# Kernel tuning notes

Measured on AMD Instinct MI355X. Metric: run time of the kernel, lower is better.

## Reference

```python
import jax, jax.numpy as jnp
import numpy as np

D = 1024
H = 16
DK = D // H


def apply_rope(x):
    # x: [B, H, T, dk]; interleaved-pair RoPE as in the torch source
    T, dim = x.shape[-2], x.shape[-1]
    inv_freq = 1.0 / (10000.0 ** (jnp.arange(0, dim, 2, dtype=x.dtype) / dim))  # [dk/2]
    pos = jnp.arange(T, dtype=x.dtype)
    sinusoid = pos[:, None] * inv_freq[None, :]  # [T, dk/2]
    sin, cos = jnp.sin(sinusoid), jnp.cos(sinusoid)
    x1, x2 = x[..., ::2], x[..., 1::2]
    rot = jnp.stack([x1 * cos - x2 * sin, x1 * sin + x2 * cos], axis=-1)
    return rot.reshape(x.shape)


def setup_inputs() -> dict:
    key = jax.random.key(0)
    k1, k2, k3, k4, k5 = jax.random.split(key, 5)
    B, T = 2, 2048
    s = 1.0 / np.sqrt(D)
    return {
        "x": jax.random.normal(k1, (B, T, D), dtype=jnp.float32),
        "W_qkv": jax.random.normal(k2, (D, 3 * D), dtype=jnp.float32) * s,
        "b_qkv": jnp.zeros((3 * D,), dtype=jnp.float32),
        "W_out": jax.random.normal(k3, (D, D), dtype=jnp.float32) * s,
        "b_out": jnp.zeros((D,), dtype=jnp.float32),
    }


def reference(x, W_qkv, b_qkv, W_out, b_out):
    B, T, C = x.shape
    qkv = x @ W_qkv + b_qkv  # [B, T, 3D]
    qkv = qkv.reshape(B, T, 3, H, DK).transpose(2, 0, 3, 1, 4)  # [3, B, H, T, dk]
    q, k, v = qkv[0], qkv[1], qkv[2]
    q, k = apply_rope(q), apply_rope(k)
    scores = jnp.einsum("bhtd,bhsd->bhts", q, k) / jnp.sqrt(jnp.asarray(DK, x.dtype))
    causal = jnp.tril(jnp.ones((T, T), dtype=bool))
    scores = jnp.where(causal, scores, jnp.asarray(-1e9, x.dtype))
    probs = jax.nn.softmax(scores, axis=-1)
    attn = jnp.einsum("bhts,bhsd->bhtd", probs, v)  # [B, H, T, dk]
    out = attn.transpose(0, 2, 1, 3).reshape(B, T, C)  # b h t d -> b t (h d)
    return out @ W_out + b_out
```

## Files before the change

kernel.cpp:

```cpp
#include <hip/hip_runtime.h>
#include <math.h>

#define DMODEL 1024
#define NHEAD  16
#define HDK    64
#define BATCH  2
#define SEQ    2048
#define MROWS  (BATCH*SEQ)
#define NQKV   (3*DMODEL)
#define LOG2_10000 13.287712379549449f
#define INV2PI 0.15915494309189535f
#define SCALE_LOG2E 0.1803368801111137f
#define M_FIX 8.0f

typedef __attribute__((ext_vector_type(8))) short bf16x8;
typedef __attribute__((ext_vector_type(4))) float f32x4;

__device__ __forceinline__ short f2bf(float f) {
    union { float f; unsigned u; } v; v.f = f;
    unsigned r = v.u + 0x7fffu + ((v.u >> 16) & 1u);
    return (short)(r >> 16);
}

__device__ __forceinline__ float fast_exp2(float x) {
#if __has_builtin(__builtin_amdgcn_exp2f)
    return __builtin_amdgcn_exp2f(x);
#else
    return exp2f(x);
#endif
}

__device__ __forceinline__ void gld_lds16(const short* g, short* l) {
    __builtin_amdgcn_global_load_lds(
        (const __attribute__((address_space(1))) void*)g,
        (__attribute__((address_space(3))) void*)l, 16, 0, 0);
}

__global__ __launch_bounds__(256) void prep_kernel(
    const float* __restrict__ x, const float* __restrict__ wqkv,
    const float* __restrict__ wout,
    short* __restrict__ xb, short* __restrict__ wqkv_t, short* __restrict__ wout_t)
{
    __shared__ short tile[32][33];
    const int tid = threadIdx.x;
    if (blockIdx.x < 2048) {
        const int i = (blockIdx.x * 256 + tid) * 8;
        float4 a = *(const float4*)(x + i);
        float4 b = *(const float4*)(x + i + 4);
        bf16x8 o;
        o[0] = f2bf(a.x); o[1] = f2bf(a.y); o[2] = f2bf(a.z); o[3] = f2bf(a.w);
        o[4] = f2bf(b.x); o[5] = f2bf(b.y); o[6] = f2bf(b.z); o[7] = f2bf(b.w);
        *(bf16x8*)(xb + i) = o;
        return;
    }
    const int bx = blockIdx.x - 2048;
    int nx = bx & 127;
    const int ky = bx >> 7;
    const float* in; short* out; int N;
    if (nx < 96) { in = wqkv; out = wqkv_t; N = NQKV; }
    else         { in = wout; out = wout_t; N = DMODEL; nx -= 96; }
    const int tx = tid & 31, ty = tid >> 5;
    const int n0 = nx * 32, k0 = ky * 32;
    #pragma unroll
    for (int i = 0; i < 32; i += 8)
        tile[ty + i][tx] = f2bf(in[(size_t)(k0 + ty + i) * N + n0 + tx]);
    __syncthreads();
    #pragma unroll
    for (int i = 0; i < 32; i += 8)
        out[(size_t)(n0 + ty + i) * DMODEL + k0 + tx] = tile[tx][ty + i];
}

__global__ __launch_bounds__(256) void qkv_gemm_kernel(
    const short* __restrict__ xb, const short* __restrict__ Wt,
    const float* __restrict__ bias,
    short* __restrict__ qd, short* __restrict__ kd, short* __restrict__ vtb)
{
    __shared__ __align__(16) short As[128 * 32];
    __shared__ __align__(16) short Bs[128 * 32];
    const int tid = threadIdx.x;
    const int lane = tid & 63, wave = tid >> 6;
    const int wm = wave & 1, wn = wave >> 1;
    const int l15 = lane & 15, quad = lane >> 4;
    const int n0 = blockIdx.x * 128, m0 = blockIdx.y * 128;
    const int srow = lane >> 2, sc = lane & 3;

    const short* gA1 = xb + (size_t)(m0 + wave * 32 + srow) * DMODEL + sc * 8;
    const short* gA2 = gA1 + (size_t)16 * DMODEL;
    const short* gB1 = Wt + (size_t)(n0 + wave * 32 + srow) * DMODEL + sc * 8;
    const short* gB2 = gB1 + (size_t)16 * DMODEL;
    short* lA1 = As + (wave * 32) * 32;
    short* lA2 = As + (wave * 32 + 16) * 32;
    short* lB1 = Bs + (wave * 32) * 32;
    short* lB2 = Bs + (wave * 32 + 16) * 32;

    f32x4 zero = {0.f, 0.f, 0.f, 0.f};
    f32x4 acc[4][4];
    #pragma unroll
    for (int i = 0; i < 4; ++i)
        #pragma unroll
        for (int j = 0; j < 4; ++j) acc[i][j] = zero;

    for (int k0 = 0; k0 < DMODEL; k0 += 32) {
        __syncthreads();
        gld_lds16(gA1 + k0, lA1);
        gld_lds16(gA2 + k0, lA2);
        gld_lds16(gB1 + k0, lB1);
        gld_lds16(gB2 + k0, lB2);
        __syncthreads();
        bf16x8 af[4], bfr[4];
        #pragma unroll
        for (int i = 0; i < 4; ++i)
            af[i] = *(const bf16x8*)&As[(wm * 64 + i * 16 + l15) * 32 + quad * 8];
        #pragma unroll
        for (int j = 0; j < 4; ++j)
            bfr[j] = *(const bf16x8*)&Bs[(wn * 64 + j * 16 + l15) * 32 + quad * 8];
        #pragma unroll
        for (int i = 0; i < 4; ++i)
            #pragma unroll
            for (int j = 0; j < 4; ++j)
                acc[i][j] = __builtin_amdgcn_mfma_f32_16x16x32_bf16(af[i], bfr[j], acc[i][j], 0, 0, 0);
    }

    const int which = n0 >> 10;
    float biasv[4], invf[4];
    int hh[4], dd[4];
    #pragma unroll
    for (int j = 0; j < 4; ++j) {
        const int n = n0 + wn * 64 + j * 16 + l15;
        biasv[j] = bias[n];
        hh[j] = (n & 1023) >> 6;
        dd[j] = n & 63;
        invf[j] = INV2PI * exp2f(-((float)(dd[j] & ~1) / 64.f) * LOG2_10000);
    }
    #pragma unroll
    for (int i = 0; i < 4; ++i) {
        #pragma unroll
        for (int r = 0; r < 4; ++r) {
            const int m = m0 + wm * 64 + i * 16 + quad * 4 + r;
            const int b = m >> 11, t = m & (SEQ - 1);
            #pragma unroll
            for (int j = 0; j < 4; ++j) {
                float val = acc[i][j][r] + biasv[j];
                if (which < 2) {
                    const float rev = (float)t * invf[j];
                    const float fr = rev - floorf(rev);
                    const float s = __builtin_amdgcn_sinf(fr);
                    const float c = __builtin_amdgcn_cosf(fr);
                    const float partner = __shfl_xor(val, 1);
                    val = (lane & 1) ? (partner * s + val * c) : (val * c - partner * s);
                    short* dst = (which == 0) ? qd : kd;
                    dst[((size_t)(b * NHEAD + hh[j]) * SEQ + t) * HDK + dd[j]] = f2bf(val);
                } else {
                    vtb[((size_t)(b * NHEAD + hh[j]) * HDK + dd[j]) * SEQ + t] = f2bf(val);
                }
            }
        }
    }
}

__global__ __launch_bounds__(256) void attn_mfma_kernel(
    const short* __restrict__ qd, const short* __restrict__ kd,
    const short* __restrict__ vt, short* __restrict__ od)
{
    __shared__ __align__(16) short Ks[2][2][64 * 32];
    __shared__ __align__(16) short Vs[2][2][64 * 32];
    __shared__ __align__(16) short Ps[4][16][72];
    const int tid = threadIdx.x, lane = tid & 63, w = tid >> 6;
    const int l15 = lane & 15, quad = lane >> 4;
    const int id = (int)blockIdx.x;
    const int c = id & 7, kk = id >> 3;
    const int qp = kk & 15, jj = kk >> 4;
    const int hb = c + 8 * jj;
    const int h = hb & 15, b = hb >> 4;
    const size_t base = ((size_t)(b * NHEAD + h)) * SEQ * HDK;
    const int srow = tid >> 2, sc = tid & 3;
    const int lofs = tid * 8;
    f32x4 zero = {0.f, 0.f, 0.f, 0.f};

    const int qtile[2] = { qp, 31 - qp };
    const short* kp0 = kd + base + (size_t)srow * HDK + sc * 8;
    const short* vp0 = vt + base + (size_t)srow * SEQ + sc * 8;
    const short* kp1 = kp0 + (size_t)64 * HDK;
    const short* vp1 = vp0 + 64;

    #pragma unroll 1
    for (int qi = 0; qi < 2; ++qi) {
        const int q0 = qtile[qi] * 64;
        bf16x8 qf[2];
        {
            const short* qrow = qd + base + (size_t)(q0 + w * 16 + l15) * HDK;
            qf[0] = *(const bf16x8*)(qrow + quad * 8);
            qf[1] = *(const bf16x8*)(qrow + 32 + quad * 8);
        }
        float l_acc[4] = {0.f, 0.f, 0.f, 0.f};
        f32x4 o[4];
        #pragma unroll
        for (int j = 0; j < 4; ++j) o[j] = zero;

        const int nkt = q0 / 64 + 1;
        const int npair = (nkt + 1) >> 1;

        bf16x8 rk[2][2], rv[2][2];
        rk[0][0] = *(const bf16x8*)kp0; rk[0][1] = *(const bf16x8*)(kp0 + 32);
        rv[0][0] = *(const bf16x8*)vp0; rv[0][1] = *(const bf16x8*)(vp0 + 32);
        rk[1][0] = *(const bf16x8*)kp1; rk[1][1] = *(const bf16x8*)(kp1 + 32);
        rv[1][0] = *(const bf16x8*)vp1; rv[1][1] = *(const bf16x8*)(vp1 + 32);

        for (int p = 0; p < npair; ++p) {
            __syncthreads();
            *(bf16x8*)&Ks[0][0][lofs] = rk[0][0]; *(bf16x8*)&Ks[0][1][lofs] = rk[0][1];
            *(bf16x8*)&Vs[0][0][lofs] = rv[0][0]; *(bf16x8*)&Vs[0][1][lofs] = rv[0][1];
            *(bf16x8*)&Ks[1][0][lofs] = rk[1][0]; *(bf16x8*)&Ks[1][1][lofs] = rk[1][1];
            *(bf16x8*)&Vs[1][0][lofs] = rv[1][0]; *(bf16x8*)&Vs[1][1][lofs] = rv[1][1];
            __syncthreads();
            if (p + 1 < npair) {
                const int sn = (2 * p + 2) * 64;
                const short* kn = kd + base + (size_t)(sn + srow) * HDK + sc * 8;
                const short* vn = vt + base + (size_t)srow * SEQ + sn + sc * 8;
                rk[0][0] = *(const bf16x8*)kn; rk[0][1] = *(const bf16x8*)(kn + 32);
                rv[0][0] = *(const bf16x8*)vn; rv[0][1] = *(const bf16x8*)(vn + 32);
                const short* kn2 = kn + (size_t)64 * HDK;
                const short* vn2 = vn + 64;
                rk[1][0] = *(const bf16x8*)kn2; rk[1][1] = *(const bf16x8*)(kn2 + 32);
                rv[1][0] = *(const bf16x8*)vn2; rv[1][1] = *(const bf16x8*)(vn2 + 32);
            } else if (qi == 0) {
                rk[0][0] = *(const bf16x8*)kp0; rk[0][1] = *(const bf16x8*)(kp0 + 32);
                rv[0][0] = *(const bf16x8*)vp0; rv[0][1] = *(const bf16x8*)(vp0 + 32);
                rk[1][0] = *(const bf16x8*)kp1; rk[1][1] = *(const bf16x8*)(kp1 + 32);
                rv[1][0] = *(const bf16x8*)vp1; rv[1][1] = *(const bf16x8*)(vp1 + 32);
            }

            #pragma unroll
            for (int tt = 0; tt < 2; ++tt) {
                const int kt = 2 * p + tt;
                if (tt == 1 && kt >= nkt) break;
                f32x4 sacc[4];
                #pragma unroll
                for (int j = 0; j < 4; ++j) {
                    bf16x8 kf0 = *(const bf16x8*)&Ks[tt][0][(j * 16 + l15) * 32 + quad * 8];
                    bf16x8 kf1 = *(const bf16x8*)&Ks[tt][1][(j * 16 + l15) * 32 + quad * 8];
                    sacc[j] = __builtin_amdgcn_mfma_f32_16x16x32_bf16(qf[0], kf0, zero, 0, 0, 0);
                    sacc[j] = __builtin_amdgcn_mfma_f32_16x16x32_bf16(qf[1], kf1, sacc[j], 0, 0, 0);
                }
                if (kt == nkt - 1) {
                    const int s0 = kt * 64;
                    #pragma unroll
                    for (int j = 0; j < 4; ++j) {
                        const int scol = s0 + j * 16 + l15;
                        #pragma unroll
                        for (int r = 0; r < 4; ++r) {
                            const int trow = q0 + w * 16 + quad * 4 + r;
                            const float sv = sacc[j][r] * SCALE_LOG2E - M_FIX;
                            const float pv = (scol > trow) ? 0.f : fast_exp2(sv);
                            l_acc[r] += pv;
                            Ps[w][quad * 4 + r][j * 16 + l15] = f2bf(pv);
                        }
                    }
                } else {
                    #pragma unroll
                    for (int j = 0; j < 4; ++j)
                        #pragma unroll
                        for (int r = 0; r < 4; ++r) {
                            const float pv = fast_exp2(sacc[j][r] * SCALE_LOG2E - M_FIX);
                            l_acc[r] += pv;
                            Ps[w][quad * 4 + r][j * 16 + l15] = f2bf(pv);
                        }
                }
                bf16x8 pf0 = *(const bf16x8*)&Ps[w][l15][quad * 8];
                bf16x8 pf1 = *(const bf16x8*)&Ps[w][l15][32 + quad * 8];
                #pragma unroll
                for (int j = 0; j < 4; ++j) {
                    bf16x8 vf0 = *(const bf16x8*)&Vs[tt][0][(j * 16 + l15) * 32 + quad * 8];
                    bf16x8 vf1 = *(const bf16x8*)&Vs[tt][1][(j * 16 + l15) * 32 + quad * 8];
                    o[j] = __builtin_amdgcn_mfma_f32_16x16x32_bf16(pf0, vf0, o[j], 0, 0, 0);
                    o[j] = __builtin_amdgcn_mfma_f32_16x16x32_bf16(pf1, vf1, o[j], 0, 0, 0);
                }
            }
        }

        #pragma unroll
        for (int r = 0; r < 4; ++r) {
            float sr = l_acc[r];
            #pragma unroll
            for (int off = 1; off < 16; off <<= 1) sr += __shfl_xor(sr, off);
            l_acc[r] = sr;
        }
        #pragma unroll
        for (int r = 0; r < 4; ++r) {
            const float inv = 1.f / l_acc[r];
            const int t = q0 + w * 16 + quad * 4 + r;
            #pragma unroll
            for (int j = 0; j < 4; ++j)
                od[((size_t)(b * SEQ + t) * NHEAD + h) * HDK + j * 16 + l15] =
                    f2bf(o[j][r] * inv);
        }
    }
}

__global__ __launch_bounds__(256) void out_gemm_kernel(
    const short* __restrict__ Ab, const short* __restrict__ Wt,
    const float* __restrict__ bias, float* __restrict__ out)
{
    __shared__ __align__(16) short As[128 * 32];
    __shared__ __align__(16) short Bs[128 * 32];
    const int tid = threadIdx.x;
    const int lane = tid & 63, wave = tid >> 6;
    const int wm = wave & 1, wn = wave >> 1;
    const int l15 = lane & 15, quad = lane >> 4;
    const int n0 = blockIdx.x * 128, m0 = blockIdx.y * 128;
    const int srow = lane >> 2, sc = lane & 3;

    const short* gA1 = Ab + (size_t)(m0 + wave * 32 + srow) * DMODEL + sc * 8;
    const short* gA2 = gA1 + (size_t)16 * DMODEL;
    const short* gB1 = Wt + (size_t)(n0 + wave * 32 + srow) * DMODEL + sc * 8;
    const short* gB2 = gB1 + (size_t)16 * DMODEL;
    short* lA1 = As + (wave * 32) * 32;
    short* lA2 = As + (wave * 32 + 16) * 32;
    short* lB1 = Bs + (wave * 32) * 32;
    short* lB2 = Bs + (wave * 32 + 16) * 32;

    f32x4 zero = {0.f, 0.f, 0.f, 0.f};
    f32x4 acc[4][4];
    #pragma unroll
    for (int i = 0; i < 4; ++i)
        #pragma unroll
        for (int j = 0; j < 4; ++j) acc[i][j] = zero;

    for (int k0 = 0; k0 < DMODEL; k0 += 32) {
        __syncthreads();
        gld_lds16(gA1 + k0, lA1);
        gld_lds16(gA2 + k0, lA2);
        gld_lds16(gB1 + k0, lB1);
        gld_lds16(gB2 + k0, lB2);
        __syncthreads();
        bf16x8 af[4], bfr[4];
        #pragma unroll
        for (int i = 0; i < 4; ++i)
            af[i] = *(const bf16x8*)&As[(wm * 64 + i * 16 + l15) * 32 + quad * 8];
        #pragma unroll
        for (int j = 0; j < 4; ++j)
            bfr[j] = *(const bf16x8*)&Bs[(wn * 64 + j * 16 + l15) * 32 + quad * 8];
        #pragma unroll
        for (int i = 0; i < 4; ++i)
            #pragma unroll
            for (int j = 0; j < 4; ++j)
                acc[i][j] = __builtin_amdgcn_mfma_f32_16x16x32_bf16(af[i], bfr[j], acc[i][j], 0, 0, 0);
    }

    #pragma unroll
    for (int j = 0; j < 4; ++j) {
        const int n = n0 + wn * 64 + j * 16 + l15;
        const float bv = bias[n];
        #pragma unroll
        for (int i = 0; i < 4; ++i)
            #pragma unroll
            for (int r = 0; r < 4; ++r) {
                const int m = m0 + wm * 64 + i * 16 + quad * 4 + r;
                out[(size_t)m * DMODEL + n] = acc[i][j][r] + bv;
            }
    }
}

extern "C" void kernel_launch(void* const* d_in, const int* in_sizes, int n_in,
                              void* d_out, int out_size, void* d_ws, size_t ws_size,
                              hipStream_t stream) {
    const float* x    = (const float*)d_in[0];
    const float* Wqkv = (const float*)d_in[1];
    const float* bqkv = (const float*)d_in[2];
    const float* Wout = (const float*)d_in[3];
    const float* bout = (const float*)d_in[4];
    float* out = (float*)d_out;

    short* ws = (short*)d_ws;
    short* xb     = ws;
    short* wqkv_t = xb + (size_t)4 * 1024 * 1024;
    short* wout_t = wqkv_t + (size_t)3 * 1024 * 1024;
    short* qd     = wout_t + (size_t)1024 * 1024;
    short* kd     = qd + (size_t)4 * 1024 * 1024;
    short* vtb    = kd + (size_t)4 * 1024 * 1024;
    short* attn   = vtb + (size_t)4 * 1024 * 1024;

    prep_kernel<<<2048 + 4096, 256, 0, stream>>>(x, Wqkv, Wout, xb, wqkv_t, wout_t);

    qkv_gemm_kernel<<<dim3(NQKV / 128, MROWS / 128), 256, 0, stream>>>(
        xb, wqkv_t, bqkv, qd, kd, vtb);

    attn_mfma_kernel<<<512, 256, 0, stream>>>(qd, kd, vtb, attn);

    out_gemm_kernel<<<dim3(DMODEL / 128, MROWS / 128), 256, 0, stream>>>(
        attn, wout_t, bout, out);
}
```

Measured before the change: 198.3 us.

## Split paired causal q-tiles into one tile per block, swizzle P tile

The attention kernel previously gave each block two query tiles (qp and 31-qp) so per-block causal work was balanced. Now each block handles one query tile, and the grid doubles to 1024 blocks ordered longest-first so the hardware scheduler can balance the work. The P staging buffer in shared memory drops its padding and uses an XOR swizzle to avoid bank conflicts. The trade-off is more blocks with uneven per-block work and repeated Q/K setup, in exchange for more parallelism and better tail behaviour.

Measured after the change: 202.6 us. +2.2%, slower.

```diff
diff --git a/kernel.cpp b/kernel.cpp
--- a/kernel.cpp
+++ b/kernel.cpp
@@ -164,12 +164,13 @@
 {
     __shared__ __align__(16) short Ks[2][2][64 * 32];
     __shared__ __align__(16) short Vs[2][2][64 * 32];
-    __shared__ __align__(16) short Ps[4][16][72];
+    __shared__ __align__(16) short Ps[4][16][64];
     const int tid = threadIdx.x, lane = tid & 63, w = tid >> 6;
     const int l15 = lane & 15, quad = lane >> 4;
     const int id = (int)blockIdx.x;
-    const int c = id & 7, kk = id >> 3;
-    const int qp = kk & 15, jj = kk >> 4;
+    const int c = id & 7, kblk = id >> 3;
+    const int qt = 31 - (kblk & 31);
+    const int jj = kblk >> 5;
     const int hb = c + 8 * jj;
     const int h = hb & 15, b = hb >> 4;
     const size_t base = ((size_t)(b * NHEAD + h)) * SEQ * HDK;
@@ -177,123 +178,118 @@
     const int lofs = tid * 8;
     f32x4 zero = {0.f, 0.f, 0.f, 0.f};
 
-    const int qtile[2] = { qp, 31 - qp };
     const short* kp0 = kd + base + (size_t)srow * HDK + sc * 8;
     const short* vp0 = vt + base + (size_t)srow * SEQ + sc * 8;
     const short* kp1 = kp0 + (size_t)64 * HDK;
     const short* vp1 = vp0 + 64;
 
-    #pragma unroll 1
-    for (int qi = 0; qi < 2; ++qi) {
-        const int q0 = qtile[qi] * 64;
-        bf16x8 qf[2];
-        {
-            const short* qrow = qd + base + (size_t)(q0 + w * 16 + l15) * HDK;
-            qf[0] = *(const bf16x8*)(qrow + quad * 8);
-            qf[1] = *(const bf16x8*)(qrow + 32 + quad * 8);
+    const int q0 = qt * 64;
+    bf16x8 qf[2];
+    {
+        const short* qrow = qd + base + (size_t)(q0 + w * 16 + l15) * HDK;
+        qf[0] = *(const bf16x8*)(qrow + quad * 8);
+        qf[1] = *(const bf16x8*)(qrow + 32 + quad * 8);
+    }
+    float l_acc[4] = {0.f, 0.f, 0.f, 0.f};
+    f32x4 o[4];
+    #pragma unroll
+    for (int j = 0; j < 4; ++j) o[j] = zero;
+
+    const int nkt = qt + 1;
+    const int npair = (nkt + 1) >> 1;
+
+    bf16x8 rk[2][2], rv[2][2];
+    rk[0][0] = *(const bf16x8*)kp0; rk[0][1] = *(const bf16x8*)(kp0 + 32);
+    rv[0][0] = *(const bf16x8*)vp0; rv[0][1] = *(const bf16x8*)(vp0 + 32);
+    rk[1][0] = *(const bf16x8*)kp1; rk[1][1] = *(const bf16x8*)(kp1 + 32);
+    rv[1][0] = *(const bf16x8*)vp1; rv[1][1] = *(const bf16x8*)(vp1 + 32);
+
+    for (int p = 0; p < npair; ++p) {
+        __syncthreads();
+        *(bf16x8*)&Ks[0][0][lofs] = rk[0][0]; *(bf16x8*)&Ks[0][1][lofs] = rk[0][1];
+        *(bf16x8*)&Vs[0][0][lofs] = rv[0][0]; *(bf16x8*)&Vs[0][1][lofs] = rv[0][1];
+        *(bf16x8*)&Ks[1][0][lofs] = rk[1][0]; *(bf16x8*)&Ks[1][1][lofs] = rk[1][1];
+        *(bf16x8*)&Vs[1][0][lofs] = rv[1][0]; *(bf16x8*)&Vs[1][1][lofs] = rv[1][1];
+        __syncthreads();
+        if (p + 1 < npair) {
+            const int sn = (2 * p + 2) * 64;
+            const short* kn = kd + base + (size_t)(sn + srow) * HDK + sc * 8;
+            const short* vn = vt + base + (size_t)srow * SEQ + sn + sc * 8;
+            rk[0][0] = *(const bf16x8*)kn; rk[0][1] = *(const bf16x8*)(kn + 32);
+            rv[0][0] = *(const bf16x8*)vn; rv[0][1] = *(const bf16x8*)(vn + 32);
+            const short* kn2 = kn + (size_t)64 * HDK;
+            const short* vn2 = vn + 64;
+            rk[1][0] = *(const bf16x8*)kn2; rk[1][1] = *(const bf16x8*)(kn2 + 32);
+            rv[1][0] = *(const bf16x8*)vn2; rv[1][1] = *(const bf16x8*)(vn2 + 32);
         }
-        float l_acc[4] = {0.f, 0.f, 0.f, 0.f};
-        f32x4 o[4];
-        #pragma unroll
-        for (int j = 0; j < 4; ++j) o[j] = zero;
-
-        const int nkt = q0 / 64 + 1;
-        const int npair = (nkt + 1) >> 1;
-
-        bf16x8 rk[2][2], rv[2][2];
-        rk[0][0] = *(const bf16x8*)kp0; rk[0][1] = *(const bf16x8*)(kp0 + 32);
-        rv[0][0] = *(const bf16x8*)vp0; rv[0][1] = *(const bf16x8*)(vp0 + 32);
-        rk[1][0] = *(const bf16x8*)kp1; rk[1][1] = *(const bf16x8*)(kp1 + 32);
-        rv[1][0] = *(const bf16x8*)vp1; rv[1][1] = *(const bf16x8*)(vp1 + 32);
-
-        for (int p = 0; p < npair; ++p) {
-            __syncthreads();
-            *(bf16x8*)&Ks[0][0][lofs] = rk[0][0]; *(bf16x8*)&Ks[0][1][lofs] = rk[0][1];
-            *(bf16x8*)&Vs[0][0][lofs] = rv[0][0]; *(bf16x8*)&Vs[0][1][lofs] = rv[0][1];
-            *(bf16x8*)&Ks[1][0][lofs] = rk[1][0]; *(bf16x8*)&Ks[1][1][lofs] = rk[1][1];
-            *(bf16x8*)&Vs[1][0][lofs] = rv[1][0]; *(bf16x8*)&Vs[1][1][lofs] = rv[1][1];
-            __syncthreads();
-            if (p + 1 < npair) {
-                const int sn = (2 * p + 2) * 64;
-                const short* kn = kd + base + (size_t)(sn + srow) * HDK + sc * 8;
-                const short* vn = vt + base + (size_t)srow * SEQ + sn + sc * 8;
-                rk[0][0] = *(const bf16x8*)kn; rk[0][1] = *(const bf16x8*)(kn + 32);
-                rv[0][0] = *(const bf16x8*)vn; rv[0][1] = *(const bf16x8*)(vn + 32);
-                const short* kn2 = kn + (size_t)64 * HDK;
-                const short* vn2 = vn + 64;
-                rk[1][0] = *(const bf16x8*)kn2; rk[1][1] = *(const bf16x8*)(kn2 + 32);
-                rv[1][0] = *(const bf16x8*)vn2; rv[1][1] = *(const bf16x8*)(vn2 + 32);
-            } else if (qi == 0) {
-                rk[0][0] = *(const bf16x8*)kp0; rk[0][1] = *(const bf16x8*)(kp0 + 32);
-                rv[0][0] = *(const bf16x8*)vp0; rv[0][1] = *(const bf16x8*)(vp0 + 32);
-                rk[1][0] = *(const bf16x8*)kp1; rk[1][1] = *(const bf16x8*)(kp1 + 32);
-                rv[1][0] = *(const bf16x8*)vp1; rv[1][1] = *(const bf16x8*)(vp1 + 32);
-            }
-
-            #pragma unroll
-            for (int tt = 0; tt < 2; ++tt) {
-                const int kt = 2 * p + tt;
-                if (tt == 1 && kt >= nkt) break;
-                f32x4 sacc[4];
+
+        #pragma unroll
+        for (int tt = 0; tt < 2; ++tt) {
+            const int kt = 2 * p + tt;
+            if (tt == 1 && kt >= nkt) break;
+            f32x4 sacc[4];
+            #pragma unroll
+            for (int j = 0; j < 4; ++j) {
+                bf16x8 kf0 = *(const bf16x8*)&Ks[tt][0][(j * 16 + l15) * 32 + quad * 8];
+                bf16x8 kf1 = *(const bf16x8*)&Ks[tt][1][(j * 16 + l15) * 32 + quad * 8];
+                sacc[j] = __builtin_amdgcn_mfma_f32_16x16x32_bf16(qf[0], kf0, zero, 0, 0, 0);
+                sacc[j] = __builtin_amdgcn_mfma_f32_16x16x32_bf16(qf[1], kf1, sacc[j], 0, 0, 0);
+            }
+            if (kt == nkt - 1) {
+                const int s0 = kt * 64;
                 #pragma unroll
                 for (int j = 0; j < 4; ++j) {
-                    bf16x8 kf0 = *(const bf16x8*)&Ks[tt][0][(j * 16 + l15) * 32 + quad * 8];
-                    bf16x8 kf1 = *(const bf16x8*)&Ks[tt][1][(j * 16 + l15) * 32 + quad * 8];
-                    sacc[j] = __builtin_amdgcn_mfma_f32_16x16x32_bf16(qf[0], kf0, zero, 0, 0, 0);
-                    sacc[j] = __builtin_amdgcn_mfma_f32_16x16x32_bf16(qf[1], kf1, sacc[j], 0, 0, 0);
+                    const int scol = s0 + j * 16 + l15;
+                    #pragma unroll
+                    for (int r = 0; r < 4; ++r) {
+                        const int trow = q0 + w * 16 + quad * 4 + r;
+                        const float sv = sacc[j][r] * SCALE_LOG2E - M_FIX;
+                        const float pv = (scol > trow) ? 0.f : fast_exp2(sv);
+                        l_acc[r] += pv;
+                        const int pr = quad * 4 + r;
+                        const int sw = (j * 2 + (l15 >> 3)) ^ (pr & 7);
+                        Ps[w][pr][sw * 8 + (l15 & 7)] = f2bf(pv);
+                    }
                 }
-                if (kt == nkt - 1) {
-                    const int s0 = kt * 64;
+            } else {
+                #pragma unroll
+                for (int j = 0; j < 4; ++j)
                     #pragma unroll
-                    for (int j = 0; j < 4; ++j) {
-                        const int scol = s0 + j * 16 + l15;
-                        #pragma unroll
-                        for (int r = 0; r < 4; ++r) {
-                            const int trow = q0 + w * 16 + quad * 4 + r;
-                            const float sv = sacc[j][r] * SCALE_LOG2E - M_FIX;
-                            const float pv = (scol > trow) ? 0.f : fast_exp2(sv);
-                            l_acc[r] += pv;
-                            Ps[w][quad * 4 + r][j * 16 + l15] = f2bf(pv);
-                        }
+                    for (int r = 0; r < 4; ++r) {
+                        const float pv = fast_exp2(sacc[j][r] * SCALE_LOG2E - M_FIX);
+                        l_acc[r] += pv;
+                        const int pr = quad * 4 + r;
+                        const int sw = (j * 2 + (l15 >> 3)) ^ (pr & 7);
+                        Ps[w][pr][sw * 8 + (l15 & 7)] = f2bf(pv);
                     }
-                } else {
-                    #pragma unroll
-                    for (int j = 0; j < 4; ++j)
-                        #pragma unroll
-                        for (int r = 0; r < 4; ++r) {
-                            const float pv = fast_exp2(sacc[j][r] * SCALE_LOG2E - M_FIX);
-                            l_acc[r] += pv;
-                            Ps[w][quad * 4 + r][j * 16 + l15] = f2bf(pv);
-                        }
-                }
-                bf16x8 pf0 = *(const bf16x8*)&Ps[w][l15][quad * 8];
-                bf16x8 pf1 = *(const bf16x8*)&Ps[w][l15][32 + quad * 8];
-                #pragma unroll
-                for (int j = 0; j < 4; ++j) {
-                    bf16x8 vf0 = *(const bf16x8*)&Vs[tt][0][(j * 16 + l15) * 32 + quad * 8];
-                    bf16x8 vf1 = *(const bf16x8*)&Vs[tt][1][(j * 16 + l15) * 32 + quad * 8];
-                    o[j] = __builtin_amdgcn_mfma_f32_16x16x32_bf16(pf0, vf0, o[j], 0, 0, 0);
-                    o[j] = __builtin_amdgcn_mfma_f32_16x16x32_bf16(pf1, vf1, o[j], 0, 0, 0);
-                }
+            }
+            bf16x8 pf0 = *(const bf16x8*)&Ps[w][l15][(quad ^ (l15 & 7)) * 8];
+            bf16x8 pf1 = *(const bf16x8*)&Ps[w][l15][((4 + quad) ^ (l15 & 7)) * 8];
+            #pragma unroll
+            for (int j = 0; j < 4; ++j) {
+                bf16x8 vf0 = *(const bf16x8*)&Vs[tt][0][(j * 16 + l15) * 32 + quad * 8];
+                bf16x8 vf1 = *(const bf16x8*)&Vs[tt][1][(j * 16 + l15) * 32 + quad * 8];
+                o[j] = __builtin_amdgcn_mfma_f32_16x16x32_bf16(pf0, vf0, o[j], 0, 0, 0);
+                o[j] = __builtin_amdgcn_mfma_f32_16x16x32_bf16(pf1, vf1, o[j], 0, 0, 0);
             }
         }
-
-        #pragma unroll
-        for (int r = 0; r < 4; ++r) {
-            float sr = l_acc[r];
-            #pragma unroll
-            for (int off = 1; off < 16; off <<= 1) sr += __shfl_xor(sr, off);
-            l_acc[r] = sr;
-        }
-        #pragma unroll
-        for (int r = 0; r < 4; ++r) {
-            const float inv = 1.f / l_acc[r];
-            const int t = q0 + w * 16 + quad * 4 + r;
-            #pragma unroll
-            for (int j = 0; j < 4; ++j)
-                od[((size_t)(b * SEQ + t) * NHEAD + h) * HDK + j * 16 + l15] =
-                    f2bf(o[j][r] * inv);
-        }
+    }
+
+    #pragma unroll
+    for (int r = 0; r < 4; ++r) {
+        float sr = l_acc[r];
+        #pragma unroll
+        for (int off = 1; off < 16; off <<= 1) sr += __shfl_xor(sr, off);
+        l_acc[r] = sr;
+    }
+    #pragma unroll
+    for (int r = 0; r < 4; ++r) {
+        const float inv = 1.f / l_acc[r];
+        const int t = q0 + w * 16 + quad * 4 + r;
+        #pragma unroll
+        for (int j = 0; j < 4; ++j)
+            od[((size_t)(b * SEQ + t) * NHEAD + h) * HDK + j * 16 + l15] =
+                f2bf(o[j][r] * inv);
     }
 }
 
@@ -385,7 +381,7 @@
     qkv_gemm_kernel<<<dim3(NQKV / 128, MROWS / 128), 256, 0, stream>>>(
         xb, wqkv_t, bqkv, qd, kd, vtb);
 
-    attn_mfma_kernel<<<512, 256, 0, stream>>>(qd, kd, vtb, attn);
+    attn_mfma_kernel<<<1024, 256, 0, stream>>>(qd, kd, vtb, attn);
 
     out_gemm_kernel<<<dim3(DMODEL / 128, MROWS / 128), 256, 0, stream>>>(
         attn, wout_t, bout, out);
```
